# Kernel tuning notes

Hardware: AMD Instinct MI355X
Metric: run time of the kernel (lower is better)

## Reference

```python
import jax, jax.numpy as jnp
import numpy as np

P = 2            # power (even positive int)
TEMPERATURE = 1.0
SCALE = 1.0 / np.sqrt(64.0)  # sqrt(head_dim) scaling
EPS = 1e-6


def setup_inputs() -> dict:
    key = jax.random.key(0)
    kq, kk, kv = jax.random.split(key, 3)
    shape = (4, 16, 2048, 64)  # (B, H, N, head_dim)
    return {
        "q": jax.random.normal(kq, shape, dtype=jnp.float32),
        "k": jax.random.normal(kk, shape, dtype=jnp.float32),
        "v": jax.random.normal(kv, shape, dtype=jnp.float32),
    }


def reference(q, k, v):
    # logits = q @ k^T * scale / temperature : (B, H, N, N)
    logits = jnp.einsum("bhnd,bhmd->bhnm", q, k) * (SCALE / TEMPERATURE)
    attn = logits ** P
    attn = attn / (attn.sum(axis=-1, keepdims=True) + EPS)
    return jnp.einsum("bhnm,bhmd->bhnd", attn, v)
```

## Files before the change

kernel.cpp:

```cpp
#include <hip/hip_runtime.h>

#define N_CTX 2048
#define DHEAD 64
#define SCALE_F 0.125f
#define EPS_F 1e-6f
#define KT 64
#define NITER (N_CTX / KT)
#define QBLK 128

typedef __attribute__((ext_vector_type(8))) short short8;
typedef __attribute__((ext_vector_type(4))) short short4v;
typedef __attribute__((ext_vector_type(4))) float float4v;
typedef __attribute__((ext_vector_type(2))) unsigned uint2v;
typedef __attribute__((ext_vector_type(4))) unsigned uint4v;

#if defined(__HIP_DEVICE_COMPILE__) && __has_builtin(__builtin_amdgcn_cvt_pk_bf16_f32)
typedef __attribute__((ext_vector_type(2))) __bf16 bf16x2;
__device__ __forceinline__ unsigned pack2(float a, float b) {
    union { bf16x2 v; unsigned u; } x;
    x.v = __builtin_amdgcn_cvt_pk_bf16_f32(a, b);
    return x.u;
}
#else
__device__ __forceinline__ unsigned bf1(float f) {
    union { float f; unsigned u; } x; x.f = f;
    return (x.u + 0x7FFFu + ((x.u >> 16) & 1u)) >> 16;
}
__device__ __forceinline__ unsigned pack2(float a, float b) {
    return bf1(a) | (bf1(b) << 16);
}
#endif

#if defined(__HIP_DEVICE_COMPILE__)
  #if __has_builtin(__builtin_amdgcn_mfma_f32_16x16x16bf16_1k)
    #define MFMA16(a, b, c) __builtin_amdgcn_mfma_f32_16x16x16bf16_1k(a, b, c, 0, 0, 0)
  #elif __has_builtin(__builtin_amdgcn_mfma_f32_16x16x16_bf16_1k)
    #define MFMA16(a, b, c) __builtin_amdgcn_mfma_f32_16x16x16_bf16_1k(a, b, c, 0, 0, 0)
  #else
    __device__ __forceinline__ float4v mfma16_asm(short4v a, short4v b, float4v c) {
        asm volatile("v_mfma_f32_16x16x16_bf16 %0, %1, %2, %0"
                     : "+v"(c) : "v"(a), "v"(b));
        return c;
    }
    #define MFMA16(a, b, c) mfma16_asm(a, b, c)
  #endif
#else
  #define MFMA16(a, b, c) (c)
#endif


__global__ __launch_bounds__(256, 3)
void powsm_attn(const float* __restrict__ qg, const float* __restrict__ kg,
                const float* __restrict__ vg, float* __restrict__ og)
{
    __shared__ short Ks[2][64][72];
    __shared__ short Vt[2][64][68];
    __shared__ float Dn[4][32];

    const int i     = blockIdx.x;
    const int bh    = (i & 7) * 8 + ((i >> 3) & 7);
    const int qtile = i >> 6;

    const int tid  = threadIdx.x;
    const int wave = tid >> 6;
    const int lane = tid & 63;
    const int qd   = lane >> 4;
    const int c    = lane & 15;

    const size_t base = (size_t)bh * N_CTX * DHEAD;
    const float* qp = qg + base;
    const float* kp = kg + base;
    const float* vp = vg + base;
    float*       op = og + base;

    const int qw0 = qtile * QBLK + wave * 32;

    short8 Qf[2][2];
    #pragma unroll
    for (int qt = 0; qt < 2; ++qt) {
        #pragma unroll
        for (int ks = 0; ks < 2; ++ks) {
            const float* src = qp + (size_t)(qw0 + qt*16 + c) * DHEAD + ks*32 + qd*8;
            float4v a = *(const float4v*)(src);
            float4v b = *(const float4v*)(src + 4);
            uint4v u;
            u[0] = pack2(a[0]*SCALE_F, a[1]*SCALE_F);
            u[1] = pack2(a[2]*SCALE_F, a[3]*SCALE_F);
            u[2] = pack2(b[0]*SCALE_F, b[1]*SCALE_F);
            u[3] = pack2(b[2]*SCALE_F, b[3]*SCALE_F);
            union { uint4v u; short8 s; } cv; cv.u = u;
            Qf[qt][ks] = cv.s;
        }
    }

    float4v Oacc[2][4];
    #pragma unroll
    for (int qt = 0; qt < 2; ++qt)
        #pragma unroll
        for (int nt = 0; nt < 4; ++nt)
            Oacc[qt][nt] = (float4v){0.f, 0.f, 0.f, 0.f};
    float4v dacc[2];
    dacc[0] = (float4v){0.f, 0.f, 0.f, 0.f};
    dacc[1] = (float4v){0.f, 0.f, 0.f, 0.f};

    const int sr = tid >> 4;
    const int sc = tid & 15;

    float4v pK[4], pV[4];

    #define LOAD_TILE(t)                                                        \
        do {                                                                    \
            const float* kn_ = kp + (size_t)(t) * KT * DHEAD;                   \
            const float* vn_ = vp + (size_t)(t) * KT * DHEAD;                   \
            _Pragma("unroll")                                                   \
            for (int u_ = 0; u_ < 4; ++u_)                                      \
                pK[u_] = *(const float4v*)(kn_ + (size_t)(sr + u_*16) * DHEAD + sc*4); \
            _Pragma("unroll")                                                   \
            for (int j_ = 0; j_ < 4; ++j_)                                      \
                pV[j_] = *(const float4v*)(vn_ + (size_t)(4*sr + j_) * DHEAD + sc*4);  \
        } while (0)

    #define STAGE_TILE(buf)                                                     \
        do {                                                                    \
            _Pragma("unroll")                                                   \
            for (int u_ = 0; u_ < 4; ++u_) {                                    \
                uint2v w_; w_[0] = pack2(pK[u_][0], pK[u_][1]);                 \
                           w_[1] = pack2(pK[u_][2], pK[u_][3]);                 \
                *(uint2v*)&Ks[buf][sr + u_*16][sc*4] = w_;                      \
            }                                                                   \
            _Pragma("unroll")                                                   \
            for (int kk_ = 0; kk_ < 4; ++kk_) {                                 \
                uint2v w_; w_[0] = pack2(pV[0][kk_], pV[1][kk_]);               \
                           w_[1] = pack2(pV[2][kk_], pV[3][kk_]);               \
                *(uint2v*)&Vt[buf][4*sc + kk_][4*sr] = w_;                      \
            }                                                                   \
        } while (0)

    LOAD_TILE(0);
    STAGE_TILE(0);
    LOAD_TILE(1);
    __syncthreads();

    #pragma unroll 1
    for (int kvi = 0; kvi < NITER; ++kvi) {
        const int cur = kvi & 1;

        if (kvi + 1 < NITER) STAGE_TILE(cur ^ 1);
        if (kvi + 2 < NITER) LOAD_TILE(kvi + 2);

        #pragma unroll
        for (int mt = 0; mt < 4; ++mt) {
            float4v s[2];
            s[0] = (float4v){0.f, 0.f, 0.f, 0.f};
            s[1] = (float4v){0.f, 0.f, 0.f, 0.f};
            #pragma unroll
            for (int ks = 0; ks < 2; ++ks) {
                short8 af = *(const short8*)&Ks[cur][mt*16 + c][ks*32 + qd*8];
                #pragma unroll
                for (int qt = 0; qt < 2; ++qt)
                    s[qt] = __builtin_amdgcn_mfma_f32_16x16x32_bf16(af, Qf[qt][ks], s[qt], 0, 0, 0);
            }
            short4v pa[2];
            #pragma unroll
            for (int qt = 0; qt < 2; ++qt) {
                float4v p = s[qt] * s[qt];
                dacc[qt] += p;
                union { uint2v u; short4v s; } cv;
                cv.u[0] = pack2(p[0], p[1]); cv.u[1] = pack2(p[2], p[3]);
                pa[qt] = cv.s;
            }
            #pragma unroll
            for (int nt = 0; nt < 4; ++nt) {
                short4v bf = *(const short4v*)&Vt[cur][nt*16 + c][mt*16 + qd*4];
                #pragma unroll
                for (int qt = 0; qt < 2; ++qt)
                    Oacc[qt][nt] = MFMA16(pa[qt], bf, Oacc[qt][nt]);
            }
        }
        __syncthreads();
    }

    #pragma unroll
    for (int qt = 0; qt < 2; ++qt) {
        float d = (dacc[qt][0] + dacc[qt][1]) + (dacc[qt][2] + dacc[qt][3]);
        d += __shfl_xor(d, 16);
        d += __shfl_xor(d, 32);
        if (qd == 0) Dn[wave][qt*16 + c] = d;
    }
    __syncthreads();

    #pragma unroll
    for (int qt = 0; qt < 2; ++qt) {
        #pragma unroll
        for (int r = 0; r < 4; ++r) {
            float inv = 1.0f / (Dn[wave][qt*16 + qd*4 + r] + EPS_F);
            float* dst = op + (size_t)(qw0 + qt*16 + qd*4 + r) * DHEAD + c;
            #pragma unroll
            for (int nt = 0; nt < 4; ++nt)
                dst[nt*16] = Oacc[qt][nt][r] * inv;
        }
    }
}

extern "C" void kernel_launch(void* const* d_in, const int* in_sizes, int n_in,
                              void* d_out, int out_size, void* d_ws, size_t ws_size,
                              hipStream_t stream) {
    const float* q = (const float*)d_in[0];
    const float* k = (const float*)d_in[1];
    const float* v = (const float*)d_in[2];
    float* out = (float*)d_out;
    dim3 grid((N_CTX / QBLK) * 64, 1, 1);
    powsm_attn<<<grid, dim3(256, 1, 1), 0, stream>>>(q, k, v, out);
}
```

Baseline: 217.2 us.

## Swizzle K and transposed-V shared tiles with XOR layout, raise occupancy hint

Replaces the padded shared-memory layouts for K and transposed V with unpadded 64x64 tiles using XOR swizzles on 8- and 4-element chunks. This cuts LDS bank conflicts without padding, and the smaller footprint allows launch bounds of 4 blocks per CU. The V global load mapping also changes so that each thread's transposed writes land on the swizzled layout. In exchange, address arithmetic and register use go up, and the higher occupancy target may force register spills.

```diff
diff --git a/kernel.cpp b/kernel.cpp
--- a/kernel.cpp
+++ b/kernel.cpp
@@ -49,12 +49,12 @@
 #endif
 
 
-__global__ __launch_bounds__(256, 3)
+__global__ __launch_bounds__(256, 4)
 void powsm_attn(const float* __restrict__ qg, const float* __restrict__ kg,
                 const float* __restrict__ vg, float* __restrict__ og)
 {
-    __shared__ short Ks[2][64][72];
-    __shared__ short Vt[2][64][68];
+    __shared__ short Ks[2 * 64 * 64];
+    __shared__ short Vt[2 * 64 * 64];
     __shared__ float Dn[4][32];
 
     const int i     = blockIdx.x;
@@ -103,8 +103,28 @@
     dacc[0] = (float4v){0.f, 0.f, 0.f, 0.f};
     dacc[1] = (float4v){0.f, 0.f, 0.f, 0.f};
 
+    int afBase[2];
+    #pragma unroll
+    for (int ks = 0; ks < 2; ++ks)
+        afBase[ks] = c*64 + ((4*ks + qd) ^ (c & 7))*8;
+    int vBase[4];
+    #pragma unroll
+    for (int mt = 0; mt < 4; ++mt)
+        vBase[mt] = c*64 + ((2*mt + (qd >> 1)) ^ ((c >> 1) & 7))*8
+                  + ((qd & 1) ^ (c & 1))*4;
+
     const int sr = tid >> 4;
     const int sc = tid & 15;
+    const int kwBase = sr*64 + ((sc >> 1) ^ (sr & 7))*8 + (sc & 1)*4;
+    const int X = tid >> 4;
+    const int Y = tid & 15;
+    int vwBase[4];
+    #pragma unroll
+    for (int kk = 0; kk < 4; ++kk) {
+        const int d = 4*X + kk;
+        vwBase[kk] = d*64 + ((Y >> 1) ^ ((d >> 1) & 7))*8
+                   + ((Y & 1) ^ (d & 1))*4;
+    }
 
     float4v pK[4], pV[4];
 
@@ -117,7 +137,7 @@
                 pK[u_] = *(const float4v*)(kn_ + (size_t)(sr + u_*16) * DHEAD + sc*4); \
             _Pragma("unroll")                                                   \
             for (int j_ = 0; j_ < 4; ++j_)                                      \
-                pV[j_] = *(const float4v*)(vn_ + (size_t)(4*sr + j_) * DHEAD + sc*4);  \
+                pV[j_] = *(const float4v*)(vn_ + (size_t)(4*Y + j_) * DHEAD + X*4);    \
         } while (0)
 
     #define STAGE_TILE(buf)                                                     \
@@ -126,13 +146,13 @@
             for (int u_ = 0; u_ < 4; ++u_) {                                    \
                 uint2v w_; w_[0] = pack2(pK[u_][0], pK[u_][1]);                 \
                            w_[1] = pack2(pK[u_][2], pK[u_][3]);                 \
-                *(uint2v*)&Ks[buf][sr + u_*16][sc*4] = w_;                      \
+                *(uint2v*)&Ks[(buf)*4096 + kwBase + u_*1024] = w_;              \
             }                                                                   \
             _Pragma("unroll")                                                   \
             for (int kk_ = 0; kk_ < 4; ++kk_) {                                 \
                 uint2v w_; w_[0] = pack2(pV[0][kk_], pV[1][kk_]);               \
                            w_[1] = pack2(pV[2][kk_], pV[3][kk_]);               \
-                *(uint2v*)&Vt[buf][4*sc + kk_][4*sr] = w_;                      \
+                *(uint2v*)&Vt[(buf)*4096 + vwBase[kk_]] = w_;                   \
             }                                                                   \
         } while (0)
 
@@ -155,7 +175,7 @@
             s[1] = (float4v){0.f, 0.f, 0.f, 0.f};
             #pragma unroll
             for (int ks = 0; ks < 2; ++ks) {
-                short8 af = *(const short8*)&Ks[cur][mt*16 + c][ks*32 + qd*8];
+                short8 af = *(const short8*)&Ks[cur*4096 + afBase[ks] + mt*1024];
                 #pragma unroll
                 for (int qt = 0; qt < 2; ++qt)
                     s[qt] = __builtin_amdgcn_mfma_f32_16x16x32_bf16(af, Qf[qt][ks], s[qt], 0, 0, 0);
@@ -171,7 +191,7 @@
             }
             #pragma unroll
             for (int nt = 0; nt < 4; ++nt) {
-                short4v bf = *(const short4v*)&Vt[cur][nt*16 + c][mt*16 + qd*4];
+                short4v bf = *(const short4v*)&Vt[cur*4096 + vBase[mt] + nt*1024];
                 #pragma unroll
                 for (int qt = 0; qt < 2; ++qt)
                     Oacc[qt][nt] = MFMA16(pa[qt], bf, Oacc[qt][nt]);
```

After: 226.0 us. +4.1%, slower.
